# Optimization experiments

Hardware: AMD Instinct MI355X
Metric: run time of the kernel (lower is better)

The kernel has to match this reference:

```python
import jax, jax.numpy as jnp
import numpy as np

N = 50000   # nodes
E = 800000  # edges (avg degree 16)
D = 128     # in = hidden = out channels (residual path active)
EPS = 1e-5  # BatchNorm eps


def setup_inputs() -> dict:
    key = jax.random.key(0)
    ks = jax.random.split(key, 24)
    sc = 1.0 / np.sqrt(D)
    inp = {
        "x": jax.random.normal(ks[0], (N, D), jnp.float32),
        "W1": jax.random.normal(ks[1], (D, D), jnp.float32) * sc,
        "b1": jnp.zeros((D,), jnp.float32),
        "g1": 1.0 + 0.1 * jax.random.normal(ks[2], (D,), jnp.float32),
        "be1": 0.1 * jax.random.normal(ks[3], (D,), jnp.float32),
        "m1": 0.1 * jax.random.normal(ks[4], (D,), jnp.float32),
        "v1": 0.5 + jax.random.uniform(ks[5], (D,), jnp.float32),
        "W2": jax.random.normal(ks[6], (D, D), jnp.float32) * sc,
        "b2": jnp.zeros((D,), jnp.float32),
        "g2": 1.0 + 0.1 * jax.random.normal(ks[7], (D,), jnp.float32),
        "be2": 0.1 * jax.random.normal(ks[8], (D,), jnp.float32),
        "m2": 0.1 * jax.random.normal(ks[9], (D,), jnp.float32),
        "v2": 0.5 + jax.random.uniform(ks[10], (D,), jnp.float32),
        "W3": jax.random.normal(ks[11], (D, D), jnp.float32) * sc,
        "b3": jnp.zeros((D,), jnp.float32),
        "src": jax.random.randint(ks[12], (E,), 0, N, jnp.int32),
        "dst": jax.random.randint(ks[13], (E,), 0, N, jnp.int32),
    }
    return inp


def _gcn_conv(x, W, b, src, dst):
    # PyG GCNConv: add self-loops, symmetric D^{-1/2}(A+I)D^{-1/2} normalization.
    h = x @ W                                              # [N, C]
    deg = jax.ops.segment_sum(jnp.ones((E,), x.dtype), dst, num_segments=N) + 1.0
    dinv = jax.lax.rsqrt(deg)                              # [N]
    coef = dinv[src] * dinv[dst]                           # [E]
    agg = jax.ops.segment_sum(h[src] * coef[:, None], dst, num_segments=N)
    agg = agg + h * (dinv * dinv)[:, None]                 # self-loop term
    return agg + b


def _bn(x, g, be, m, v):
    # eval-mode BatchNorm1d with running stats
    return (x - m) * jax.lax.rsqrt(v + EPS) * g + be


def reference(x, W1, b1, g1, be1, m1, v1, W2, b2, g2, be2, m2, v2, W3, b3, src, dst):
    x_res = x
    h = jax.nn.relu(_bn(_gcn_conv(x, W1, b1, src, dst), g1, be1, m1, v1))
    h = jax.nn.relu(_bn(_gcn_conv(h, W2, b2, src, dst), g2, be2, m2, v2))
    h = _gcn_conv(h, W3, b3, src, dst)
    return h + x_res  # in_channels == out_channels -> residual active
```

## Files before the change

### kernel.cpp

```cpp
#include <hip/hip_runtime.h>
#include <hip/hip_bf16.h>


#define GCN_N 50000
#define GCN_E 800000
#define GCN_D 128
#define NBK 16
#define NREP 8
#define SEGCAP 16384

using bf16x8 = __attribute__((ext_vector_type(8))) short;
using f32x4  = __attribute__((ext_vector_type(4))) float;

__device__ __forceinline__ float bflo(unsigned u) { return __uint_as_float(u << 16); }
__device__ __forceinline__ float bfhi(unsigned u) { return __uint_as_float(u & 0xffff0000u); }
__device__ __forceinline__ unsigned f2bf(float f) {
    unsigned u = __float_as_uint(f);
    return (u + 0x7fffu + ((u >> 16) & 1u)) >> 16;
}

__global__ __launch_bounds__(256) void prep_all(const float* __restrict__ x,
                                                unsigned short* __restrict__ xb,
                                                const float* __restrict__ W1,
                                                const float* __restrict__ W2,
                                                const float* __restrict__ W3,
                                                unsigned short* __restrict__ wt1,
                                                unsigned short* __restrict__ wt2,
                                                unsigned short* __restrict__ wt3,
                                                int* __restrict__ cnt,
                                                int* __restrict__ bcur) {
    int gid = blockIdx.x * 256 + threadIdx.x;
    int i = gid * 8;
    if (i + 7 < GCN_N * GCN_D) {
        float4 f0 = *(const float4*)&x[i];
        float4 f1 = *(const float4*)&x[i + 4];
        uint4 o;
        o.x = f2bf(f0.x) | (f2bf(f0.y) << 16);
        o.y = f2bf(f0.z) | (f2bf(f0.w) << 16);
        o.z = f2bf(f1.x) | (f2bf(f1.y) << 16);
        o.w = f2bf(f1.z) | (f2bf(f1.w) << 16);
        *(uint4*)&xb[i] = o;
    }
    if (gid < GCN_N) cnt[gid] = 0;
    if (gid < NBK * NREP) bcur[gid] = 0;
    if (gid < GCN_D * GCN_D) {
        int nn = gid >> 7, k = gid & 127;
        wt1[gid] = (unsigned short)f2bf(W1[k * 128 + nn]);
        wt2[gid] = (unsigned short)f2bf(W2[k * 128 + nn]);
        wt3[gid] = (unsigned short)f2bf(W3[k * 128 + nn]);
    }
}

__global__ __launch_bounds__(256) void fillA(const int* __restrict__ src,
                                             const int* __restrict__ dst,
                                             int* __restrict__ cnt,
                                             int* __restrict__ bcur,
                                             int2* __restrict__ pairs, int nE) {
    __shared__ int lcnt[NBK];
    __shared__ int lbase[NBK];
    int tid = threadIdx.x;
    if (tid < NBK) lcnt[tid] = 0;
    __syncthreads();
    int e = blockIdx.x * 256 + tid;
    int rep = blockIdx.x & (NREP - 1);
    int s = 0, d = 0, b = 0, off = 0;
    bool valid = e < nE;
    if (valid) {
        s = src[e];
        d = dst[e];
        atomicAdd(&cnt[d], 1);
        b = d >> 12;
        off = atomicAdd(&lcnt[b], 1);
    }
    __syncthreads();
    if (tid < NBK)
        lbase[tid] = lcnt[tid] ? atomicAdd(&bcur[tid * NREP + rep], lcnt[tid]) : 0;
    __syncthreads();
    if (valid)
        pairs[(size_t)(b * NREP + rep) * SEGCAP + lbase[b] + off] = make_int2(s, d);
}

__global__ __launch_bounds__(256) void fillB(const int2* __restrict__ pairs,
                                             const int* __restrict__ bcur,
                                             const int* __restrict__ row_ptr,
                                             int* __restrict__ cur,
                                             int* __restrict__ esrc) {
    int b = blockIdx.x & (NBK - 1);
    int j = blockIdx.x >> 4;
    int tid = threadIdx.x;
    #pragma unroll
    for (int r = 0; r < NREP; ++r) {
        int cr = bcur[b * NREP + r];
        const int2* seg = pairs + (size_t)(b * NREP + r) * SEGCAP;
        for (int i = j * 256 + tid; i < cr; i += 32 * 256) {
            int2 p = seg[i];
            int pos = row_ptr[p.y] + atomicAdd(&cur[p.y], 1);
            esrc[pos] = p.x;
        }
    }
}

__global__ __launch_bounds__(256) void block_reduce(const int* __restrict__ cnt,
                                                    int* __restrict__ bsum, int n) {
    int tid = threadIdx.x, lane = tid & 63, wid = tid >> 6;
    int i0 = blockIdx.x * 1024 + tid * 4;
    int s = 0;
    #pragma unroll
    for (int q = 0; q < 4; ++q)
        if (i0 + q < n) s += cnt[i0 + q];
    #pragma unroll
    for (int off = 32; off >= 1; off >>= 1) s += __shfl_xor(s, off);
    __shared__ int ws[4];
    if (lane == 0) ws[wid] = s;
    __syncthreads();
    if (tid == 0) bsum[blockIdx.x] = ws[0] + ws[1] + ws[2] + ws[3];
}

__global__ void scan_bsums(const int* __restrict__ bsum, int* __restrict__ boff,
                           int nb, int* __restrict__ row_last) {
    int lane = threadIdx.x;
    int v = (lane < nb) ? bsum[lane] : 0;
    int sc = v;
    #pragma unroll
    for (int off = 1; off < 64; off <<= 1) {
        int t = __shfl_up(sc, off);
        if (lane >= off) sc += t;
    }
    if (lane < nb) boff[lane] = sc - v;
    if (lane == 63) *row_last = sc;
}

__global__ __launch_bounds__(256) void scan_apply(const int* __restrict__ cnt_in,
                                                  const int* __restrict__ boff,
                                                  int* __restrict__ row_ptr,
                                                  float* __restrict__ dinv,
                                                  int* __restrict__ cnt_zero, int n) {
    __shared__ int wsum[4];
    int tid = threadIdx.x, lane = tid & 63, wid = tid >> 6;
    int i0 = blockIdx.x * 1024 + tid * 4;
    int a0 = 0, a1 = 0, a2 = 0, a3 = 0;
    if (i0 + 0 < n) a0 = cnt_in[i0 + 0];
    if (i0 + 1 < n) a1 = cnt_in[i0 + 1];
    if (i0 + 2 < n) a2 = cnt_in[i0 + 2];
    if (i0 + 3 < n) a3 = cnt_in[i0 + 3];
    int tsum = a0 + a1 + a2 + a3;
    int sc = tsum;
    #pragma unroll
    for (int off = 1; off < 64; off <<= 1) {
        int t = __shfl_up(sc, off);
        if (lane >= off) sc += t;
    }
    if (lane == 63) wsum[wid] = sc;
    __syncthreads();
    int woff = 0;
    #pragma unroll
    for (int w = 0; w < 4; ++w)
        if (w < wid) woff += wsum[w];
    int excl = boff[blockIdx.x] + woff + (sc - tsum);
    if (i0 + 0 < n) { row_ptr[i0 + 0] = excl;                dinv[i0 + 0] = rsqrtf((float)a0 + 1.f); cnt_zero[i0 + 0] = 0; }
    if (i0 + 1 < n) { row_ptr[i0 + 1] = excl + a0;           dinv[i0 + 1] = rsqrtf((float)a1 + 1.f); cnt_zero[i0 + 1] = 0; }
    if (i0 + 2 < n) { row_ptr[i0 + 2] = excl + a0 + a1;      dinv[i0 + 2] = rsqrtf((float)a2 + 1.f); cnt_zero[i0 + 2] = 0; }
    if (i0 + 3 < n) { row_ptr[i0 + 3] = excl + a0 + a1 + a2; dinv[i0 + 3] = rsqrtf((float)a3 + 1.f); cnt_zero[i0 + 3] = 0; }
}

__global__ void prep_bn(const float* __restrict__ b1, const float* __restrict__ g1,
                        const float* __restrict__ be1, const float* __restrict__ m1,
                        const float* __restrict__ v1, float* __restrict__ scale1,
                        float* __restrict__ shift1,
                        const float* __restrict__ b2, const float* __restrict__ g2,
                        const float* __restrict__ be2, const float* __restrict__ m2,
                        const float* __restrict__ v2, float* __restrict__ scale2,
                        float* __restrict__ shift2) {
    int c = threadIdx.x;
    if (blockIdx.x == 0) {
        float s = g1[c] * rsqrtf(v1[c] + 1e-5f);
        scale1[c] = s;
        shift1[c] = (b1[c] - m1[c]) * s + be1[c];
    } else {
        float s = g2[c] * rsqrtf(v2[c] + 1e-5f);
        scale2[c] = s;
        shift2[c] = (b2[c] - m2[c]) * s + be2[c];
    }
}

__global__ __launch_bounds__(256) void mm_mfma(const unsigned short* __restrict__ A,
                                               const unsigned short* __restrict__ Wt,
                                               const float* __restrict__ dinv,
                                               unsigned short* __restrict__ hb, int n) {
    __shared__ unsigned short Cs[64][136];
    int tid = threadIdx.x;
    int w = tid >> 6, l = tid & 63;
    int lg = l >> 4, li = l & 15;
    int row0 = blockIdx.x * 64;

    int arow = row0 + w * 16 + li;
    int arow_c = min(arow, n - 1);
    const unsigned short* ap = A + (size_t)arow_c * GCN_D + lg * 8;
    bf16x8 a[4];
    #pragma unroll
    for (int k0 = 0; k0 < 4; ++k0) a[k0] = *(const bf16x8*)(ap + k0 * 32);

    f32x4 acc[8];
    #pragma unroll
    for (int t = 0; t < 8; ++t) acc[t] = (f32x4){0.f, 0.f, 0.f, 0.f};

    #pragma unroll
    for (int t = 0; t < 8; ++t) {
        const unsigned short* bp = Wt + (size_t)(t * 16 + li) * GCN_D + lg * 8;
        #pragma unroll
        for (int k0 = 0; k0 < 4; ++k0) {
            bf16x8 b = *(const bf16x8*)(bp + k0 * 32);
            acc[t] = __builtin_amdgcn_mfma_f32_16x16x32_bf16(a[k0], b, acc[t], 0, 0, 0);
        }
    }

    int crow = w * 16 + lg * 4;
    float dv[4];
    #pragma unroll
    for (int r = 0; r < 4; ++r) dv[r] = dinv[min(row0 + crow + r, n - 1)];
    #pragma unroll
    for (int t = 0; t < 8; ++t)
        #pragma unroll
        for (int r = 0; r < 4; ++r)
            Cs[crow + r][t * 16 + li] = (unsigned short)f2bf(acc[t][r] * dv[r]);
    __syncthreads();

    int orow = tid >> 2;
    int gr = row0 + orow;
    if (gr < n) {
        const unsigned short* sp = &Cs[orow][(tid & 3) * 32];
        uint4* dp = (uint4*)&hb[(size_t)gr * GCN_D + (tid & 3) * 32];
        dp[0] = *(const uint4*)(sp + 0);
        dp[1] = *(const uint4*)(sp + 8);
        dp[2] = *(const uint4*)(sp + 16);
        dp[3] = *(const uint4*)(sp + 24);
    }
}

template <int FINAL>
__global__ __launch_bounds__(256) void agg_kernel(const unsigned short* __restrict__ hb,
                                                  const int* __restrict__ row_ptr,
                                                  const int* __restrict__ esrc,
                                                  const float* __restrict__ dinv,
                                                  const float* __restrict__ scale,
                                                  const float* __restrict__ shift,
                                                  const float* __restrict__ xres,
                                                  unsigned short* __restrict__ outb,
                                                  float* __restrict__ outf, int n) {
    int wid = threadIdx.x >> 6, lane = threadIdx.x & 63;
    int node = blockIdx.x * 4 + wid;
    if (node >= n) return;
    int cc = lane * 2;
    unsigned us = *(const unsigned*)&hb[(size_t)node * GCN_D + cc];
    float aLo = bflo(us), aHi = bfhi(us);
    float bLo = 0.f, bHi = 0.f;
    int j = row_ptr[node], end = row_ptr[node + 1];
    for (; j + 8 <= end; j += 8) {
        int s0 = esrc[j + 0], s1 = esrc[j + 1], s2 = esrc[j + 2], s3 = esrc[j + 3];
        int s4 = esrc[j + 4], s5 = esrc[j + 5], s6 = esrc[j + 6], s7 = esrc[j + 7];
        unsigned u0 = *(const unsigned*)&hb[(size_t)s0 * GCN_D + cc];
        unsigned u1 = *(const unsigned*)&hb[(size_t)s1 * GCN_D + cc];
        unsigned u2 = *(const unsigned*)&hb[(size_t)s2 * GCN_D + cc];
        unsigned u3 = *(const unsigned*)&hb[(size_t)s3 * GCN_D + cc];
        unsigned u4 = *(const unsigned*)&hb[(size_t)s4 * GCN_D + cc];
        unsigned u5 = *(const unsigned*)&hb[(size_t)s5 * GCN_D + cc];
        unsigned u6 = *(const unsigned*)&hb[(size_t)s6 * GCN_D + cc];
        unsigned u7 = *(const unsigned*)&hb[(size_t)s7 * GCN_D + cc];
        aLo += bflo(u0) + bflo(u1);  aHi += bfhi(u0) + bfhi(u1);
        bLo += bflo(u2) + bflo(u3);  bHi += bfhi(u2) + bfhi(u3);
        aLo += bflo(u4) + bflo(u5);  aHi += bfhi(u4) + bfhi(u5);
        bLo += bflo(u6) + bflo(u7);  bHi += bfhi(u6) + bfhi(u7);
    }
    for (; j < end; ++j) {
        int s = esrc[j];
        unsigned u = *(const unsigned*)&hb[(size_t)s * GCN_D + cc];
        aLo += bflo(u);  aHi += bfhi(u);
    }
    float dvn = dinv[node];
    float vx = (aLo + bLo) * dvn;
    float vy = (aHi + bHi) * dvn;
    if (FINAL) {
        float2 b = *(const float2*)&scale[cc];
        float2 xr = *(const float2*)&xres[(size_t)node * GCN_D + cc];
        float2 o;
        o.x = vx + b.x + xr.x;
        o.y = vy + b.y + xr.y;
        *(float2*)&outf[(size_t)node * GCN_D + cc] = o;
    } else {
        float2 sc = *(const float2*)&scale[cc];
        float2 sh = *(const float2*)&shift[cc];
        float ox = fmaxf(vx * sc.x + sh.x, 0.f);
        float oy = fmaxf(vy * sc.y + sh.y, 0.f);
        *(unsigned*)&outb[(size_t)node * GCN_D + cc] = f2bf(ox) | (f2bf(oy) << 16);
    }
}

extern "C" void kernel_launch(void* const* d_in, const int* in_sizes, int n_in,
                              void* d_out, int out_size, void* d_ws, size_t ws_size,
                              hipStream_t stream) {
    (void)in_sizes; (void)n_in; (void)out_size; (void)ws_size;
    const int N = GCN_N, E = GCN_E, D = GCN_D;

    const float* x   = (const float*)d_in[0];
    const float* W1  = (const float*)d_in[1];
    const float* b1  = (const float*)d_in[2];
    const float* g1  = (const float*)d_in[3];
    const float* be1 = (const float*)d_in[4];
    const float* m1  = (const float*)d_in[5];
    const float* v1  = (const float*)d_in[6];
    const float* W2  = (const float*)d_in[7];
    const float* b2  = (const float*)d_in[8];
    const float* g2  = (const float*)d_in[9];
    const float* be2 = (const float*)d_in[10];
    const float* m2  = (const float*)d_in[11];
    const float* v2  = (const float*)d_in[12];
    const float* W3  = (const float*)d_in[13];
    const float* b3  = (const float*)d_in[14];
    const int* src   = (const int*)d_in[15];
    const int* dst   = (const int*)d_in[16];
    float* out = (float*)d_out;

    unsigned short* hb   = (unsigned short*)d_ws;
    unsigned short* actb = hb + (size_t)N * D;
    unsigned short* xb   = actb + (size_t)N * D;
    unsigned short* wt1  = xb + (size_t)N * D;
    unsigned short* wt2  = wt1 + D * D;
    unsigned short* wt3  = wt2 + D * D;
    float* dinv   = (float*)(wt3 + D * D);
    int* cnt      = (int*)(dinv + N);
    int* row_ptr  = cnt + N;
    int* esrc     = row_ptr + (N + 2);
    float* scale1 = (float*)(esrc + E);
    float* shift1 = scale1 + D;
    float* scale2 = shift1 + D;
    float* shift2 = scale2 + D;
    int* bsum     = (int*)(shift2 + D);
    int* boff     = bsum + 64;
    int* bcur     = boff + 64;
    int2* pairs   = (int2*)(bcur + NBK * NREP);

    const int NB = (N + 1023) / 1024;

    prep_all<<<(N * D) / (256 * 8), 256, 0, stream>>>(x, xb, W1, W2, W3,
                                                      wt1, wt2, wt3, cnt, bcur);
    fillA<<<(E + 255) / 256, 256, 0, stream>>>(src, dst, cnt, bcur, pairs, E);
    block_reduce<<<NB, 256, 0, stream>>>(cnt, bsum, N);
    scan_bsums<<<1, 64, 0, stream>>>(bsum, boff, NB, &row_ptr[N]);
    scan_apply<<<NB, 256, 0, stream>>>(cnt, boff, row_ptr, dinv, cnt, N);
    fillB<<<32 * NBK, 256, 0, stream>>>(pairs, bcur, row_ptr, cnt, esrc);
    prep_bn<<<2, D, 0, stream>>>(b1, g1, be1, m1, v1, scale1, shift1,
                                 b2, g2, be2, m2, v2, scale2, shift2);

    int mm_grid = (N + 63) / 64;
    int agg_grid = (N + 3) / 4;

    mm_mfma<<<mm_grid, 256, 0, stream>>>(xb, wt1, dinv, hb, N);
    agg_kernel<0><<<agg_grid, 256, 0, stream>>>(hb, row_ptr, esrc, dinv,
                                                scale1, shift1, nullptr, actb, nullptr, N);
    mm_mfma<<<mm_grid, 256, 0, stream>>>(actb, wt2, dinv, hb, N);
    agg_kernel<0><<<agg_grid, 256, 0, stream>>>(hb, row_ptr, esrc, dinv,
                                                scale2, shift2, nullptr, actb, nullptr, N);
    mm_mfma<<<mm_grid, 256, 0, stream>>>(actb, wt3, dinv, hb, N);
    agg_kernel<1><<<agg_grid, 256, 0, stream>>>(hb, row_ptr, esrc, dinv,
                                                b3, nullptr, x, nullptr, out, N);
}
```

Baseline: 434.4 us.

## Batch edge bucketing through LDS staging and move degree histogram into bucket pass

fillA now processes 2048 edges per block, counts them per destination bucket in shared memory, stages them in LDS sorted by bucket, and writes contiguous runs into a single segment per bucket (no replicas). The per-edge global atomicAdd for degree counting moves out of fillA into a new histB kernel that walks each bucket, so atomics hit a localized range of destinations. This targets scattered global writes and contended atomics, at the cost of an extra kernel launch, a second pass over the pairs buffer, and larger fixed-capacity segments.

```diff
diff --git a/kernel.cpp b/kernel.cpp
--- a/kernel.cpp
+++ b/kernel.cpp
@@ -6,8 +6,8 @@
 #define GCN_E 800000
 #define GCN_D 128
 #define NBK 16
-#define NREP 8
-#define SEGCAP 16384
+#define SEGCAP 73728
+#define FA_BATCH 2048
 
 using bf16x8 = __attribute__((ext_vector_type(8))) short;
 using f32x4  = __attribute__((ext_vector_type(4))) float;
@@ -42,7 +42,7 @@
         *(uint4*)&xb[i] = o;
     }
     if (gid < GCN_N) cnt[gid] = 0;
-    if (gid < NBK * NREP) bcur[gid] = 0;
+    if (gid < NBK) bcur[gid] = 0;
     if (gid < GCN_D * GCN_D) {
         int nn = gid >> 7, k = gid & 127;
         wt1[gid] = (unsigned short)f2bf(W1[k * 128 + nn]);
@@ -53,31 +53,58 @@
 
 __global__ __launch_bounds__(256) void fillA(const int* __restrict__ src,
                                              const int* __restrict__ dst,
-                                             int* __restrict__ cnt,
                                              int* __restrict__ bcur,
                                              int2* __restrict__ pairs, int nE) {
-    __shared__ int lcnt[NBK];
-    __shared__ int lbase[NBK];
+    __shared__ int lcnt[NBK], lpre[NBK], lbase[NBK], lpos[NBK];
+    __shared__ int2 stage[FA_BATCH];
     int tid = threadIdx.x;
+    int base = blockIdx.x * FA_BATCH;
     if (tid < NBK) lcnt[tid] = 0;
     __syncthreads();
-    int e = blockIdx.x * 256 + tid;
-    int rep = blockIdx.x & (NREP - 1);
-    int s = 0, d = 0, b = 0, off = 0;
-    bool valid = e < nE;
-    if (valid) {
-        s = src[e];
-        d = dst[e];
-        atomicAdd(&cnt[d], 1);
-        b = d >> 12;
-        off = atomicAdd(&lcnt[b], 1);
-    }
-    __syncthreads();
-    if (tid < NBK)
-        lbase[tid] = lcnt[tid] ? atomicAdd(&bcur[tid * NREP + rep], lcnt[tid]) : 0;
-    __syncthreads();
-    if (valid)
-        pairs[(size_t)(b * NREP + rep) * SEGCAP + lbase[b] + off] = make_int2(s, d);
+    int s[8], d[8], b[8];
+    bool v[8];
+    #pragma unroll
+    for (int q = 0; q < 8; ++q) {
+        int e = base + q * 256 + tid;
+        v[q] = e < nE;
+        s[q] = v[q] ? src[e] : 0;
+        d[q] = v[q] ? dst[e] : 0;
+        b[q] = d[q] >> 12;
+        if (v[q]) atomicAdd(&lcnt[b[q]], 1);
+    }
+    __syncthreads();
+    if (tid < NBK) {
+        int pre = 0;
+        for (int k = 0; k < tid; ++k) pre += lcnt[k];
+        lpre[tid] = pre;
+        lpos[tid] = pre;
+        lbase[tid] = lcnt[tid] ? atomicAdd(&bcur[tid], lcnt[tid]) : 0;
+    }
+    __syncthreads();
+    #pragma unroll
+    for (int q = 0; q < 8; ++q)
+        if (v[q]) {
+            int off = atomicAdd(&lpos[b[q]], 1);
+            stage[off] = make_int2(s[q], d[q]);
+        }
+    __syncthreads();
+    int tot = lpre[NBK - 1] + lcnt[NBK - 1];
+    for (int i = tid; i < tot; i += 256) {
+        int2 p = stage[i];
+        int bb = p.y >> 12;
+        pairs[(size_t)bb * SEGCAP + lbase[bb] + (i - lpre[bb])] = p;
+    }
+}
+
+__global__ __launch_bounds__(256) void histB(const int2* __restrict__ pairs,
+                                             const int* __restrict__ bcur,
+                                             int* __restrict__ cnt) {
+    int b = blockIdx.x & (NBK - 1);
+    int j = blockIdx.x >> 4;
+    int cr = bcur[b];
+    const int2* seg = pairs + (size_t)b * SEGCAP;
+    for (int i = j * 256 + threadIdx.x; i < cr; i += 24 * 256)
+        atomicAdd(&cnt[seg[i].y], 1);
 }
 
 __global__ __launch_bounds__(256) void fillB(const int2* __restrict__ pairs,
@@ -87,16 +114,12 @@
                                              int* __restrict__ esrc) {
     int b = blockIdx.x & (NBK - 1);
     int j = blockIdx.x >> 4;
-    int tid = threadIdx.x;
-    #pragma unroll
-    for (int r = 0; r < NREP; ++r) {
-        int cr = bcur[b * NREP + r];
-        const int2* seg = pairs + (size_t)(b * NREP + r) * SEGCAP;
-        for (int i = j * 256 + tid; i < cr; i += 32 * 256) {
-            int2 p = seg[i];
-            int pos = row_ptr[p.y] + atomicAdd(&cur[p.y], 1);
-            esrc[pos] = p.x;
-        }
+    int cr = bcur[b];
+    const int2* seg = pairs + (size_t)b * SEGCAP;
+    for (int i = j * 256 + threadIdx.x; i < cr; i += 24 * 256) {
+        int2 p = seg[i];
+        int pos = row_ptr[p.y] + atomicAdd(&cur[p.y], 1);
+        esrc[pos] = p.x;
     }
 }
 
@@ -337,17 +360,18 @@
     int* bsum     = (int*)(shift2 + D);
     int* boff     = bsum + 64;
     int* bcur     = boff + 64;
-    int2* pairs   = (int2*)(bcur + NBK * NREP);
+    int2* pairs   = (int2*)(bcur + 64);
 
     const int NB = (N + 1023) / 1024;
 
     prep_all<<<(N * D) / (256 * 8), 256, 0, stream>>>(x, xb, W1, W2, W3,
                                                       wt1, wt2, wt3, cnt, bcur);
-    fillA<<<(E + 255) / 256, 256, 0, stream>>>(src, dst, cnt, bcur, pairs, E);
+    fillA<<<(E + FA_BATCH - 1) / FA_BATCH, 256, 0, stream>>>(src, dst, bcur, pairs, E);
+    histB<<<24 * NBK, 256, 0, stream>>>(pairs, bcur, cnt);
     block_reduce<<<NB, 256, 0, stream>>>(cnt, bsum, N);
     scan_bsums<<<1, 64, 0, stream>>>(bsum, boff, NB, &row_ptr[N]);
     scan_apply<<<NB, 256, 0, stream>>>(cnt, boff, row_ptr, dinv, cnt, N);
-    fillB<<<32 * NBK, 256, 0, stream>>>(pairs, bcur, row_ptr, cnt, esrc);
+    fillB<<<24 * NBK, 256, 0, stream>>>(pairs, bcur, row_ptr, cnt, esrc);
     prep_bn<<<2, D, 0, stream>>>(b1, g1, be1, m1, v1, scale1, shift1,
                                  b2, g2, be2, m2, v2, scale2, shift2);
 
```

Measured after the change: 388.1 us. -10.6%, faster.
